# Optimization experiments

Measured on AMD Instinct MI355X. Metric: run time of the kernel, lower is better.

The kernel has to match this reference:

```python
import jax, jax.numpy as jnp
import numpy as np

MARGIN = 0.25
GAMMA = 256.0
NEG_FILL = -1e9  # finite mask value; logits are bounded by ~gamma*2.25*2, so this is safely dominated


def setup_inputs() -> dict:
    key = jax.random.key(0)
    k1, k2 = jax.random.split(key)
    embeddings = jax.random.normal(k1, (8192, 128), dtype=jnp.float32)
    labels = jax.random.randint(k2, (8192,), 0, 512)
    return {"embeddings": embeddings, "labels": labels}


def reference(embeddings, labels):
    B = embeddings.shape[0]
    # L2-normalize rows (F.normalize eps=1e-12)
    norm = jnp.maximum(jnp.linalg.norm(embeddings, axis=1, keepdims=True), 1e-12)
    e = embeddings / norm
    sim = e @ e.T  # [B, B]

    eq = labels[:, None] == labels[None, :]
    eye = jnp.eye(B, dtype=bool)
    pos_mask = eq & ~eye
    neg_mask = (~eq) & ~eye

    sim_d = jax.lax.stop_gradient(sim)  # alphas use detached similarities
    alpha_p = jnp.maximum(1.0 + MARGIN - sim_d, 0.0)
    alpha_n = jnp.maximum(sim_d + MARGIN, 0.0)

    logit_p = -GAMMA * alpha_p * (sim - (1.0 - MARGIN))
    logit_n = GAMMA * alpha_n * (sim - MARGIN)

    # masked per-row logsumexp (finite fill keeps grads clean)
    lp = jax.scipy.special.logsumexp(jnp.where(pos_mask, logit_p, NEG_FILL), axis=1)
    ln = jax.scipy.special.logsumexp(jnp.where(neg_mask, logit_n, NEG_FILL), axis=1)

    valid = pos_mask.any(axis=1) & neg_mask.any(axis=1)
    per_row = jax.nn.softplus(jnp.where(valid, lp + ln, NEG_FILL))
    per_row = jnp.where(valid, per_row, 0.0)
    n_valid = jnp.maximum(valid.sum(), 1)
    return jnp.sum(per_row) / n_valid.astype(per_row.dtype)
```

## Files before the change

### kernel.cpp

```cpp
#include <hip/hip_runtime.h>
#include <math.h>

#define NB 8192
#define ND 128
#define NT 64
#define NTRI 2080
#define NLAB 512
#define MAXM 64

typedef unsigned short u16;
typedef unsigned int u32;
typedef __attribute__((ext_vector_type(8))) short bf16x8;
typedef __attribute__((ext_vector_type(4))) float f32x4;

#define G2 369.3299304675746f
#define NEG_C (-23.083120654223414f)
#define SENT (-1e30f)
#define LN2F 0.6931471805599453f

static __device__ __forceinline__ void gload16(const void* g, void* l) {
  __builtin_amdgcn_global_load_lds(
      (const __attribute__((address_space(1))) u32*)g,
      (__attribute__((address_space(3))) u32*)l, 16, 0, 0);
}

static __device__ __forceinline__ float fexp2(float x) {
  return __builtin_amdgcn_exp2f(x);
}

static __device__ __forceinline__ u16 f2bf(float f) {
  u32 u = __float_as_uint(f);
  u32 r = (u + 0x7FFF + ((u >> 16) & 1)) >> 16;
  return (u16)r;
}

static __device__ __forceinline__ float wave_sum_f(float v) {
  #pragma unroll
  for (int off = 1; off < 64; off <<= 1) v += __shfl_xor(v, off);
  return v;
}

__global__ __launch_bounds__(512) void k_prep(const float* __restrict__ emb,
                                              u16* __restrict__ e,
                                              int* __restrict__ counters) {
  if (blockIdx.x == 0 && threadIdx.x < 2) counters[threadIdx.x] = 0;
  const int l = threadIdx.x & 63;
  const int w = threadIdx.x >> 6;
  const int row = blockIdx.x * 8 + w;
  const float2 v = reinterpret_cast<const float2*>(emb)[(size_t)row * 64 + l];
  float ss = wave_sum_f(v.x * v.x + v.y * v.y);
  const float inv = 1.0f / fmaxf(sqrtf(ss), 1e-12f);
  ushort2 o;
  o.x = f2bf(v.x * inv);
  o.y = f2bf(v.y * inv);
  reinterpret_cast<ushort2*>(e)[(size_t)row * 64 + l] = o;
}

__global__ __launch_bounds__(256, 3) void k_mainpos(const u16* __restrict__ e,
                                                    const int* __restrict__ labels,
                                                    float* __restrict__ part,
                                                    float* __restrict__ poscorr) {
  __shared__ __align__(16) char S[33792];
  const int bid = blockIdx.x;
  const int tid = threadIdx.x;
  const int l = tid & 63;
  const int w = tid >> 6;
  const int lr_ = l & 15;
  const int lg = l >> 4;

  if (bid < NTRI) {
    int ti = (int)((129.0f - sqrtf(16641.0f - 8.0f * (float)bid)) * 0.5f);
    if (ti > NT - 1) ti = NT - 1;
    if (ti < 0) ti = 0;
    #define PRE(t) ((t) * NT - ((t) * ((t) - 1)) / 2)
    while (PRE(ti + 1) <= bid) ++ti;
    while (PRE(ti) > bid) --ti;
    const int tj = ti + (bid - PRE(ti));
    #undef PRE
    const int row0 = ti * 128;
    const int col0 = tj * 128;
    const bool diag = (ti == tj);
    char* Bh[2] = { S, S + 16384 };

    bf16x8 af[2][4];
    #pragma unroll
    for (int m = 0; m < 2; ++m)
      #pragma unroll
      for (int ks = 0; ks < 4; ++ks)
        af[m][ks] = *(const bf16x8*)(e + (size_t)(row0 + w * 32 + m * 16 + lr_) * ND +
                                     ks * 32 + lg * 8);

    #pragma unroll
    for (int i = 0; i < 4; ++i) {
      const int rr = w * 16 + i * 4 + lg;
      gload16(e + (size_t)(col0 + rr) * ND + (lr_ ^ (rr & 15)) * 8,
              Bh[0] + w * 4096 + i * 1024);
    }

    float sn[8], colp[8];
    #pragma unroll
    for (int q = 0; q < 8; ++q) { sn[q] = 0.f; colp[q] = 0.f; }

    __syncthreads();

    #pragma unroll
    for (int i = 0; i < 4; ++i) {
      const int rr = w * 16 + i * 4 + lg;
      gload16(e + (size_t)(col0 + 64 + rr) * ND + (lr_ ^ (rr & 15)) * 8,
              Bh[1] + w * 4096 + i * 1024);
    }

    #pragma unroll
    for (int h = 0; h < 2; ++h) {
      f32x4 acc[2][4];
      #pragma unroll
      for (int m = 0; m < 2; ++m)
        #pragma unroll
        for (int n = 0; n < 4; ++n)
          #pragma unroll
          for (int q = 0; q < 4; ++q) acc[m][n][q] = 0.f;

      #pragma unroll
      for (int ks = 0; ks < 4; ++ks) {
        const int kslot = (ks * 4 + lg) ^ lr_;
        bf16x8 bfr[4];
        #pragma unroll
        for (int n = 0; n < 4; ++n)
          bfr[n] = *(const bf16x8*)(Bh[h] + (n * 16 + lr_) * 256 + kslot * 16);
        #pragma unroll
        for (int m = 0; m < 2; ++m)
          #pragma unroll
          for (int n = 0; n < 4; ++n)
            acc[m][n] = __builtin_amdgcn_mfma_f32_16x16x32_bf16(af[m][ks], bfr[n],
                                                                acc[m][n], 0, 0, 0);
      }

      #pragma unroll
      for (int m = 0; m < 2; ++m) {
        #pragma unroll
        for (int n = 0; n < 4; ++n) {
          const bool dmn = diag && (w * 32 + m * 16 == h * 64 + n * 16);
          float scc = 0.f;
          #pragma unroll
          for (int j = 0; j < 4; ++j) {
            const float sv = acc[m][n][j];
            float xn = fmaf(sv * sv, G2, NEG_C);
            xn = (sv > -0.25f) ? xn : 0.f;
            if (dmn) xn = (lr_ == lg * 4 + j) ? SENT : xn;
            const float ev = fexp2(xn);
            sn[m * 4 + j] += ev;
            scc += ev;
          }
          colp[h * 4 + n] += scc;
        }
      }
      if (h == 0) __syncthreads();
    }

    #pragma unroll
    for (int q = 0; q < 8; ++q) {
      #pragma unroll
      for (int off = 1; off < 16; off <<= 1) sn[q] += __shfl_xor(sn[q], off);
    }
    if (lr_ == 0) {
      #pragma unroll
      for (int m = 0; m < 2; ++m)
        #pragma unroll
        for (int j = 0; j < 4; ++j) {
          const int row = row0 + w * 32 + m * 16 + lg * 4 + j;
          part[(size_t)tj * NB + row] = sn[m * 4 + j];
        }
    }

    if (!diag) {
      #pragma unroll
      for (int q = 0; q < 8; ++q) {
        colp[q] += __shfl_xor(colp[q], 16);
        colp[q] += __shfl_xor(colp[q], 32);
      }
      __syncthreads();
      float* colbuf = (float*)S;
      if (l < 16) {
        #pragma unroll
        for (int q = 0; q < 8; ++q)
          colbuf[w * 128 + (q >> 2) * 64 + (q & 3) * 16 + lr_] = colp[q];
      }
      __syncthreads();
      if (tid < 128) {
        const float cs_ = colbuf[tid] + colbuf[128 + tid] +
                          colbuf[256 + tid] + colbuf[384 + tid];
        part[(size_t)ti * NB + col0 + tid] = cs_;
      }
    }
  } else {
    int* lab = (int*)S;
    for (int i = tid; i < NB / 4; i += 256)
      ((int4*)lab)[i] = ((const int4*)labels)[i];
    __syncthreads();

    const int L = (bid - NTRI) * 4 + w;
    int* memL = (int*)(S + 32768) + w * MAXM;

    int cnt = 0;
    for (int base = 0; base < NB; base += 64) {
      const int lv = lab[base + l];
      const unsigned long long mk = __ballot(lv == L);
      if (lv == L) {
        const int pos = __popcll(mk & ((1ull << l) - 1));
        if (cnt + pos < MAXM) memL[cnt + pos] = base + l;
      }
      cnt += __popcll(mk);
    }
    int c = cnt > MAXM ? MAXM : cnt;
    __syncthreads();

    const int nt = (c + 15) >> 4;
    for (int rb = 0; rb < nt; ++rb) {
      const int ri = rb * 16 + lr_;
      bf16x8 af[4];
      if (ri < c) {
        const u16* src = e + (size_t)memL[ri] * ND;
        #pragma unroll
        for (int ks = 0; ks < 4; ++ks)
          af[ks] = *(const bf16x8*)(src + ks * 32 + lg * 8);
      } else {
        #pragma unroll
        for (int ks = 0; ks < 4; ++ks) af[ks] = (bf16x8)0;
      }
      float corr[4], mp[4], sp[4];
      #pragma unroll
      for (int r = 0; r < 4; ++r) { corr[r] = 0.f; mp[r] = SENT; sp[r] = 0.f; }

      for (int cb = 0; cb < nt; ++cb) {
        const int ci = cb * 16 + lr_;
        bf16x8 bfr[4];
        if (ci < c) {
          const u16* src = e + (size_t)memL[ci] * ND;
          #pragma unroll
          for (int ks = 0; ks < 4; ++ks)
            bfr[ks] = *(const bf16x8*)(src + ks * 32 + lg * 8);
        } else {
          #pragma unroll
          for (int ks = 0; ks < 4; ++ks) bfr[ks] = (bf16x8)0;
        }
        f32x4 acc;
        #pragma unroll
        for (int r = 0; r < 4; ++r) acc[r] = 0.f;
        #pragma unroll
        for (int ks = 0; ks < 4; ++ks)
          acc = __builtin_amdgcn_mfma_f32_16x16x32_bf16(af[ks], bfr[ks], acc, 0, 0, 0);

        #pragma unroll
        for (int r = 0; r < 4; ++r) {
          const int R = rb * 16 + lg * 4 + r;
          const int Cj = cb * 16 + lr_;
          const bool ok = (R < c) && (Cj < c) && (R != Cj);
          const float sv = acc[r];
          float xn = fmaf(sv * sv, G2, NEG_C);
          xn = (sv > -0.25f) ? xn : 0.f;
          corr[r] += ok ? fexp2(xn) : 0.f;
          if (ok) {
            const float t1 = 1.25f - sv;
            const float xp = G2 * fmaxf(t1, 0.f) * (t1 - 0.5f);
            if (xp > mp[r]) { sp[r] = sp[r] * fexp2(mp[r] - xp) + 1.f; mp[r] = xp; }
            else sp[r] += fexp2(xp - mp[r]);
          }
        }
      }
      #pragma unroll
      for (int r = 0; r < 4; ++r) {
        #pragma unroll
        for (int off = 1; off < 16; off <<= 1) {
          corr[r] += __shfl_xor(corr[r], off);
          const float m2 = __shfl_xor(mp[r], off), s2 = __shfl_xor(sp[r], off);
          const float M = fmaxf(mp[r], m2);
          const float t1 = sp[r] * fexp2(mp[r] - M);
          const float t2 = s2 * fexp2(m2 - M);
          mp[r] = M; sp[r] = t1 + t2;
        }
      }
      if (lr_ == 0) {
        #pragma unroll
        for (int r = 0; r < 4; ++r) {
          const int R = rb * 16 + lg * 4 + r;
          if (R < c) {
            float* o = poscorr + (size_t)memL[R] * 4;
            o[0] = mp[r]; o[1] = sp[r]; o[2] = corr[r]; o[3] = (float)(c - 1);
          }
        }
      }
    }
  }
}

__global__ __launch_bounds__(256) void k_rowsfinal(const float* __restrict__ part,
                                                   const float* __restrict__ poscorr,
                                                   float* __restrict__ bsum,
                                                   int* __restrict__ counter,
                                                   float* __restrict__ out) {
  const int bid = blockIdx.x;
  const int tid = threadIdx.x;
  const int l = tid & 63, w = tid >> 6;
  const int row = bid * 256 + tid;
  float sn = 0.f;
  #pragma unroll 8
  for (int q = 0; q < NT; ++q)
    sn += part[(size_t)q * NB + row];
  const float4 pc = *reinterpret_cast<const float4*>(poscorr + (size_t)row * 4);
  const int npi = (int)(pc.w + 0.5f);
  const bool valid = (npi > 0) && (npi < NB - 1);
  float val = 0.f;
  if (valid) {
    const float snn = fmaxf(sn - pc.z, 1e-30f);
    const float lp = LN2F * (pc.x + log2f(pc.y));
    const float ln_ = LN2F * log2f(snn);
    const float x = lp + ln_;
    val = fmaxf(x, 0.f) + log1pf(expf(-fabsf(x)));
  }
  float cnt = valid ? 1.f : 0.f;
  val = wave_sum_f(val);
  cnt = wave_sum_f(cnt);
  __shared__ float svals[4], scnts[4];
  __shared__ int lastflag;
  if (l == 0) { svals[w] = val; scnts[w] = cnt; }
  __syncthreads();
  if (tid == 0) {
    bsum[bid * 2 + 0] = svals[0] + svals[1] + svals[2] + svals[3];
    bsum[bid * 2 + 1] = scnts[0] + scnts[1] + scnts[2] + scnts[3];
    __threadfence();
    const int prev = atomicAdd(counter, 1);
    lastflag = (prev == 31);
  }
  __syncthreads();
  if (lastflag && w == 0) {
    __threadfence();
    float s = 0.f, c = 0.f;
    if (l < 32) {
      volatile const float* vb = (volatile const float*)bsum;
      s = vb[l * 2];
      c = vb[l * 2 + 1];
    }
    s = wave_sum_f(s);
    c = wave_sum_f(c);
    if (l == 0) out[0] = s / fmaxf(c, 1.f);
  }
}

extern "C" void kernel_launch(void* const* d_in, const int* in_sizes, int n_in,
                              void* d_out, int out_size, void* d_ws, size_t ws_size,
                              hipStream_t stream) {
  const float* emb = (const float*)d_in[0];
  const int* labels = (const int*)d_in[1];
  float* out = (float*)d_out;
  char* ws = (char*)d_ws;

  float* part    = (float*)(ws + 0);
  float* poscorr = (float*)(ws + 2097152);
  u16*   ebf     = (u16*)  (ws + 2228224);
  float* bsum    = (float*)(ws + 4325376);
  int*   counter = (int*)  (ws + 4325632);

  k_prep<<<NB / 8, 512, 0, stream>>>(emb, ebf, counter);
  k_mainpos<<<NTRI + NLAB / 4, 256, 0, stream>>>(ebf, labels, part, poscorr);
  k_rowsfinal<<<NB / 256, 256, 0, stream>>>(part, poscorr, bsum, counter, out);
}
```

Baseline: 46.86 us.

## Fuse L2-normalization and bf16 conversion into the similarity tile kernel

Removes the separate prep kernel, so each tile block loads fp32 embeddings, normalizes them and converts to bf16 in registers before writing its B tiles to LDS. This drops one launch and the bf16 buffer round-trip, and the async global-to-LDS loads and the mid-loop barrier go away. In exchange every tile block re-reads fp32 rows (twice the bytes) and repeats the normalization work redundantly, and the counter reset becomes a memset.

Result: slower. 57.53 us (+22.8%).

```diff
diff --git a/kernel.cpp b/kernel.cpp
--- a/kernel.cpp
+++ b/kernel.cpp
@@ -18,20 +18,13 @@
 #define SENT (-1e30f)
 #define LN2F 0.6931471805599453f
 
-static __device__ __forceinline__ void gload16(const void* g, void* l) {
-  __builtin_amdgcn_global_load_lds(
-      (const __attribute__((address_space(1))) u32*)g,
-      (__attribute__((address_space(3))) u32*)l, 16, 0, 0);
-}
-
 static __device__ __forceinline__ float fexp2(float x) {
   return __builtin_amdgcn_exp2f(x);
 }
 
-static __device__ __forceinline__ u16 f2bf(float f) {
+static __device__ __forceinline__ u32 f2bf(float f) {
   u32 u = __float_as_uint(f);
-  u32 r = (u + 0x7FFF + ((u >> 16) & 1)) >> 16;
-  return (u16)r;
+  return (u + 0x7FFF + ((u >> 16) & 1)) >> 16;
 }
 
 static __device__ __forceinline__ float wave_sum_f(float v) {
@@ -40,23 +33,50 @@
   return v;
 }
 
-__global__ __launch_bounds__(512) void k_prep(const float* __restrict__ emb,
-                                              u16* __restrict__ e,
-                                              int* __restrict__ counters) {
-  if (blockIdx.x == 0 && threadIdx.x < 2) counters[threadIdx.x] = 0;
-  const int l = threadIdx.x & 63;
-  const int w = threadIdx.x >> 6;
-  const int row = blockIdx.x * 8 + w;
-  const float2 v = reinterpret_cast<const float2*>(emb)[(size_t)row * 64 + l];
-  float ss = wave_sum_f(v.x * v.x + v.y * v.y);
-  const float inv = 1.0f / fmaxf(sqrtf(ss), 1e-12f);
-  ushort2 o;
-  o.x = f2bf(v.x * inv);
-  o.y = f2bf(v.y * inv);
-  reinterpret_cast<ushort2*>(e)[(size_t)row * 64 + l] = o;
-}
-
-__global__ __launch_bounds__(256, 3) void k_mainpos(const u16* __restrict__ e,
+static __device__ __forceinline__ void load32(const float* __restrict__ src,
+                                              int g, float v[32]) {
+  #pragma unroll
+  for (int ks = 0; ks < 4; ++ks) {
+    const float4 a = *(const float4*)(src + ks * 32 + g * 8);
+    const float4 b = *(const float4*)(src + ks * 32 + g * 8 + 4);
+    v[ks * 8 + 0] = a.x; v[ks * 8 + 1] = a.y; v[ks * 8 + 2] = a.z; v[ks * 8 + 3] = a.w;
+    v[ks * 8 + 4] = b.x; v[ks * 8 + 5] = b.y; v[ks * 8 + 6] = b.z; v[ks * 8 + 7] = b.w;
+  }
+}
+
+static __device__ __forceinline__ float inv_from_ss(float ss, int o1, int o2) {
+  ss += __shfl_xor(ss, o1);
+  ss += __shfl_xor(ss, o2);
+  return 1.0f / fmaxf(sqrtf(ss), 1e-12f);
+}
+
+static __device__ __forceinline__ float ss32(const float v[32]) {
+  float ss = 0.f;
+  #pragma unroll
+  for (int j = 0; j < 32; ++j) ss = fmaf(v[j], v[j], ss);
+  return ss;
+}
+
+static __device__ __forceinline__ void norm_frags(const float* __restrict__ src,
+                                                  int g, int o1, int o2,
+                                                  bf16x8 out[4]) {
+  float v[32];
+  load32(src, g, v);
+  const float inv = inv_from_ss(ss32(v), o1, o2);
+  #pragma unroll
+  for (int ks = 0; ks < 4; ++ks) {
+    u32 wd[4];
+    #pragma unroll
+    for (int p = 0; p < 4; ++p)
+      wd[p] = f2bf(v[ks * 8 + 2 * p] * inv) | (f2bf(v[ks * 8 + 2 * p + 1] * inv) << 16);
+    bf16x8 f;
+    #pragma unroll
+    for (int p = 0; p < 4; ++p) ((u32*)&f)[p] = wd[p];
+    out[ks] = f;
+  }
+}
+
+__global__ __launch_bounds__(256, 3) void k_mainpos(const float* __restrict__ emb,
                                                     const int* __restrict__ labels,
                                                     float* __restrict__ part,
                                                     float* __restrict__ poscorr) {
@@ -80,22 +100,33 @@
     const int row0 = ti * 128;
     const int col0 = tj * 128;
     const bool diag = (ti == tj);
-    char* Bh[2] = { S, S + 16384 };
+
+    {
+      const int srow = tid >> 2;
+      const int q = tid & 3;
+      #pragma unroll
+      for (int h = 0; h < 2; ++h) {
+        const float* src = emb + (size_t)(col0 + h * 64 + srow) * ND;
+        float v[32];
+        load32(src, q, v);
+        const float inv = inv_from_ss(ss32(v), 1, 2);
+        #pragma unroll
+        for (int ks = 0; ks < 4; ++ks) {
+          uint4 wd;
+          wd.x = f2bf(v[ks * 8 + 0] * inv) | (f2bf(v[ks * 8 + 1] * inv) << 16);
+          wd.y = f2bf(v[ks * 8 + 2] * inv) | (f2bf(v[ks * 8 + 3] * inv) << 16);
+          wd.z = f2bf(v[ks * 8 + 4] * inv) | (f2bf(v[ks * 8 + 5] * inv) << 16);
+          wd.w = f2bf(v[ks * 8 + 6] * inv) | (f2bf(v[ks * 8 + 7] * inv) << 16);
+          char* dst = S + h * 16384 + srow * 256 + (((ks * 4 + q) ^ (srow & 15)) * 16);
+          *(uint4*)dst = wd;
+        }
+      }
+    }
 
     bf16x8 af[2][4];
     #pragma unroll
     for (int m = 0; m < 2; ++m)
-      #pragma unroll
-      for (int ks = 0; ks < 4; ++ks)
-        af[m][ks] = *(const bf16x8*)(e + (size_t)(row0 + w * 32 + m * 16 + lr_) * ND +
-                                     ks * 32 + lg * 8);
-
-    #pragma unroll
-    for (int i = 0; i < 4; ++i) {
-      const int rr = w * 16 + i * 4 + lg;
-      gload16(e + (size_t)(col0 + rr) * ND + (lr_ ^ (rr & 15)) * 8,
-              Bh[0] + w * 4096 + i * 1024);
-    }
+      norm_frags(emb + (size_t)(row0 + w * 32 + m * 16 + lr_) * ND, lg, 16, 32, af[m]);
 
     float sn[8], colp[8];
     #pragma unroll
@@ -104,14 +135,8 @@
     __syncthreads();
 
     #pragma unroll
-    for (int i = 0; i < 4; ++i) {
-      const int rr = w * 16 + i * 4 + lg;
-      gload16(e + (size_t)(col0 + 64 + rr) * ND + (lr_ ^ (rr & 15)) * 8,
-              Bh[1] + w * 4096 + i * 1024);
-    }
-
-    #pragma unroll
     for (int h = 0; h < 2; ++h) {
+      const char* Bh = S + h * 16384;
       f32x4 acc[2][4];
       #pragma unroll
       for (int m = 0; m < 2; ++m)
@@ -126,7 +151,7 @@
         bf16x8 bfr[4];
         #pragma unroll
         for (int n = 0; n < 4; ++n)
-          bfr[n] = *(const bf16x8*)(Bh[h] + (n * 16 + lr_) * 256 + kslot * 16);
+          bfr[n] = *(const bf16x8*)(Bh + (n * 16 + lr_) * 256 + kslot * 16);
         #pragma unroll
         for (int m = 0; m < 2; ++m)
           #pragma unroll
@@ -154,7 +179,6 @@
           colp[h * 4 + n] += scc;
         }
       }
-      if (h == 0) __syncthreads();
     }
 
     #pragma unroll
@@ -219,10 +243,7 @@
       const int ri = rb * 16 + lr_;
       bf16x8 af[4];
       if (ri < c) {
-        const u16* src = e + (size_t)memL[ri] * ND;
-        #pragma unroll
-        for (int ks = 0; ks < 4; ++ks)
-          af[ks] = *(const bf16x8*)(src + ks * 32 + lg * 8);
+        norm_frags(emb + (size_t)memL[ri] * ND, lg, 16, 32, af);
       } else {
         #pragma unroll
         for (int ks = 0; ks < 4; ++ks) af[ks] = (bf16x8)0;
@@ -235,10 +256,7 @@
         const int ci = cb * 16 + lr_;
         bf16x8 bfr[4];
         if (ci < c) {
-          const u16* src = e + (size_t)memL[ci] * ND;
-          #pragma unroll
-          for (int ks = 0; ks < 4; ++ks)
-            bfr[ks] = *(const bf16x8*)(src + ks * 32 + lg * 8);
+          norm_frags(emb + (size_t)memL[ci] * ND, lg, 16, 32, bfr);
         } else {
           #pragma unroll
           for (int ks = 0; ks < 4; ++ks) bfr[ks] = (bf16x8)0;
@@ -356,11 +374,10 @@
 
   float* part    = (float*)(ws + 0);
   float* poscorr = (float*)(ws + 2097152);
-  u16*   ebf     = (u16*)  (ws + 2228224);
-  float* bsum    = (float*)(ws + 4325376);
-  int*   counter = (int*)  (ws + 4325632);
-
-  k_prep<<<NB / 8, 512, 0, stream>>>(emb, ebf, counter);
-  k_mainpos<<<NTRI + NLAB / 4, 256, 0, stream>>>(ebf, labels, part, poscorr);
+  float* bsum    = (float*)(ws + 2228224);
+  int*   counter = (int*)  (ws + 2228480);
+
+  hipMemsetAsync(counter, 0, 8, stream);
+  k_mainpos<<<NTRI + NLAB / 4, 256, 0, stream>>>(emb, labels, part, poscorr);
   k_rowsfinal<<<NB / 256, 256, 0, stream>>>(part, poscorr, bsum, counter, out);
 }
```

## Process four triangle tiles per block with cross-tile prefetch of B and A

Applied to the files above, without the earlier changes.

Each block of the main kernel now handles four consecutive upper-triangle tiles instead of one, so the grid shrinks from 2080 to 520 tile blocks. While the second half of one tile is computed, the next tile's first B half is staged into LDS and its A fragments are loaded into a second register set. The next tile's second B half is staged after the column-sum barrier, and the column buffer moves to a dedicated LDS region. This hides global load latency and cuts per-block launch and setup cost, but it doubles the A fragment registers, lowers launch bounds occupancy from 3 to 2, and gives coarser load balance across CUs.

Result: faster. 41.60 us (-11.2%).

```diff
diff --git a/kernel.cpp b/kernel.cpp
--- a/kernel.cpp
+++ b/kernel.cpp
@@ -5,6 +5,8 @@
 #define ND 128
 #define NT 64
 #define NTRI 2080
+#define TPB 4
+#define NTRB (NTRI / TPB)
 #define NLAB 512
 #define MAXM 64
 
@@ -38,6 +40,17 @@
   #pragma unroll
   for (int off = 1; off < 64; off <<= 1) v += __shfl_xor(v, off);
   return v;
+}
+
+static __device__ __forceinline__ int pre_(int t) { return t * NT - (t * (t - 1)) / 2; }
+static __device__ __forceinline__ void trimap(int item, int& ti, int& tj) {
+  int t = (int)((129.0f - sqrtf(16641.0f - 8.0f * (float)item)) * 0.5f);
+  if (t > NT - 1) t = NT - 1;
+  if (t < 0) t = 0;
+  while (pre_(t + 1) <= item) ++t;
+  while (pre_(t) > item) --t;
+  ti = t;
+  tj = t + (item - pre_(t));
 }
 
 __global__ __launch_bounds__(512) void k_prep(const float* __restrict__ emb,
@@ -56,11 +69,61 @@
   reinterpret_cast<ushort2*>(e)[(size_t)row * 64 + l] = o;
 }
 
-__global__ __launch_bounds__(256, 3) void k_mainpos(const u16* __restrict__ e,
+#define LOADA(AF, ROW0)                                                         \
+  _Pragma("unroll")                                                             \
+  for (int m_ = 0; m_ < 2; ++m_) {                                              \
+    _Pragma("unroll")                                                           \
+    for (int ks_ = 0; ks_ < 4; ++ks_)                                           \
+      AF[m_][ks_] = *(const bf16x8*)(e + (size_t)((ROW0) + w * 32 + m_ * 16 + lr_) * ND + ks_ * 32 + lg * 8); \
+  }
+
+#define STAGEB(BUFOFF, COL0, H)                                                 \
+  _Pragma("unroll")                                                             \
+  for (int i_ = 0; i_ < 4; ++i_) {                                              \
+    const int rr_ = w * 16 + i_ * 4 + lg;                                       \
+    gload16(e + (size_t)((COL0) + (H) * 64 + rr_) * ND + (lr_ ^ (rr_ & 15)) * 8, \
+            S + (BUFOFF) + w * 4096 + i_ * 1024);                               \
+  }
+
+#define COMPUTE_HALF(AF, BUFOFF, H, ROW0, DIAG)                                 \
+  {                                                                             \
+    f32x4 acc[2][4];                                                            \
+    _Pragma("unroll") for (int m_ = 0; m_ < 2; ++m_)                            \
+      _Pragma("unroll") for (int n_ = 0; n_ < 4; ++n_)                          \
+        _Pragma("unroll") for (int q_ = 0; q_ < 4; ++q_) acc[m_][n_][q_] = 0.f; \
+    _Pragma("unroll") for (int ks_ = 0; ks_ < 4; ++ks_) {                       \
+      const int kslot_ = (ks_ * 4 + lg) ^ lr_;                                  \
+      bf16x8 bfr[4];                                                            \
+      _Pragma("unroll") for (int n_ = 0; n_ < 4; ++n_)                          \
+        bfr[n_] = *(const bf16x8*)(S + (BUFOFF) + (n_ * 16 + lr_) * 256 + kslot_ * 16); \
+      _Pragma("unroll") for (int m_ = 0; m_ < 2; ++m_)                          \
+        _Pragma("unroll") for (int n_ = 0; n_ < 4; ++n_)                        \
+          acc[m_][n_] = __builtin_amdgcn_mfma_f32_16x16x32_bf16(AF[m_][ks_], bfr[n_], acc[m_][n_], 0, 0, 0); \
+    }                                                                           \
+    _Pragma("unroll") for (int m_ = 0; m_ < 2; ++m_) {                          \
+      _Pragma("unroll") for (int n_ = 0; n_ < 4; ++n_) {                        \
+        const bool dmn_ = (DIAG) && (w * 32 + m_ * 16 == (H) * 64 + n_ * 16);   \
+        float scc_ = 0.f;                                                       \
+        _Pragma("unroll") for (int j_ = 0; j_ < 4; ++j_) {                      \
+          const float sv_ = acc[m_][n_][j_];                                    \
+          float xn_ = fmaf(sv_ * sv_, G2, NEG_C);                               \
+          xn_ = (sv_ > -0.25f) ? xn_ : 0.f;                                     \
+          if (dmn_) xn_ = (lr_ == lg * 4 + j_) ? SENT : xn_;                    \
+          const float ev_ = fexp2(xn_);                                         \
+          sn[m_ * 4 + j_] += ev_;                                               \
+          scc_ += ev_;                                                          \
+        }                                                                       \
+        colp[(H) * 4 + n_] += scc_;                                             \
+      }                                                                         \
+    }                                                                           \
+  }
+
+__global__ __launch_bounds__(256, 2) void k_mainpos(const u16* __restrict__ e,
                                                     const int* __restrict__ labels,
                                                     float* __restrict__ part,
                                                     float* __restrict__ poscorr) {
-  __shared__ __align__(16) char S[33792];
+  __shared__ __align__(16) char S[34816];
+  float* colbuf = (float*)(S + 32768);
   const int bid = blockIdx.x;
   const int tid = threadIdx.x;
   const int l = tid & 63;
@@ -68,129 +131,78 @@
   const int lr_ = l & 15;
   const int lg = l >> 4;
 
-  if (bid < NTRI) {
-    int ti = (int)((129.0f - sqrtf(16641.0f - 8.0f * (float)bid)) * 0.5f);
-    if (ti > NT - 1) ti = NT - 1;
-    if (ti < 0) ti = 0;
-    #define PRE(t) ((t) * NT - ((t) * ((t) - 1)) / 2)
-    while (PRE(ti + 1) <= bid) ++ti;
-    while (PRE(ti) > bid) --ti;
-    const int tj = ti + (bid - PRE(ti));
-    #undef PRE
-    const int row0 = ti * 128;
-    const int col0 = tj * 128;
-    const bool diag = (ti == tj);
-    char* Bh[2] = { S, S + 16384 };
-
-    bf16x8 af[2][4];
-    #pragma unroll
-    for (int m = 0; m < 2; ++m)
-      #pragma unroll
-      for (int ks = 0; ks < 4; ++ks)
-        af[m][ks] = *(const bf16x8*)(e + (size_t)(row0 + w * 32 + m * 16 + lr_) * ND +
-                                     ks * 32 + lg * 8);
-
-    #pragma unroll
-    for (int i = 0; i < 4; ++i) {
-      const int rr = w * 16 + i * 4 + lg;
-      gload16(e + (size_t)(col0 + rr) * ND + (lr_ ^ (rr & 15)) * 8,
-              Bh[0] + w * 4096 + i * 1024);
-    }
+  if (bid < NTRB) {
+    const int item0 = bid * TPB;
+    int ti, tj;
+    trimap(item0, ti, tj);
+    int row0 = ti * 128, col0 = tj * 128;
+    bool diag = (ti == tj);
+
+    bf16x8 afA[2][4], afB[2][4];
+    LOADA(afA, row0);
+    STAGEB(0, col0, 0);
 
     float sn[8], colp[8];
     #pragma unroll
     for (int q = 0; q < 8; ++q) { sn[q] = 0.f; colp[q] = 0.f; }
 
     __syncthreads();
+    STAGEB(16384, col0, 1);
 
     #pragma unroll
-    for (int i = 0; i < 4; ++i) {
-      const int rr = w * 16 + i * 4 + lg;
-      gload16(e + (size_t)(col0 + 64 + rr) * ND + (lr_ ^ (rr & 15)) * 8,
-              Bh[1] + w * 4096 + i * 1024);
-    }
-
-    #pragma unroll
-    for (int h = 0; h < 2; ++h) {
-      f32x4 acc[2][4];
-      #pragma unroll
-      for (int m = 0; m < 2; ++m)
-        #pragma unroll
-        for (int n = 0; n < 4; ++n)
-          #pragma unroll
-          for (int q = 0; q < 4; ++q) acc[m][n][q] = 0.f;
-
-      #pragma unroll
-      for (int ks = 0; ks < 4; ++ks) {
-        const int kslot = (ks * 4 + lg) ^ lr_;
-        bf16x8 bfr[4];
-        #pragma unroll
-        for (int n = 0; n < 4; ++n)
-          bfr[n] = *(const bf16x8*)(Bh[h] + (n * 16 + lr_) * 256 + kslot * 16);
+    for (int i = 0; i < TPB; ++i) {
+      int nti = 0, ntj = 0, nrow0 = 0, ncol0 = 0;
+      bool ndiag = false;
+
+      if ((i & 1) == 0) { COMPUTE_HALF(afA, 0, 0, row0, diag); }
+      else              { COMPUTE_HALF(afB, 0, 0, row0, diag); }
+      __syncthreads();
+      if (i < TPB - 1) {
+        trimap(item0 + i + 1, nti, ntj);
+        nrow0 = nti * 128; ncol0 = ntj * 128; ndiag = (nti == ntj);
+        STAGEB(0, ncol0, 0);
+        if ((i & 1) == 0) { LOADA(afB, nrow0); }
+        else              { LOADA(afA, nrow0); }
+      }
+
+      if ((i & 1) == 0) { COMPUTE_HALF(afA, 16384, 1, row0, diag); }
+      else              { COMPUTE_HALF(afB, 16384, 1, row0, diag); }
+
+      #pragma unroll
+      for (int q = 0; q < 8; ++q) {
+        #pragma unroll
+        for (int off = 1; off < 16; off <<= 1) sn[q] += __shfl_xor(sn[q], off);
+      }
+      if (lr_ == 0) {
         #pragma unroll
         for (int m = 0; m < 2; ++m)
           #pragma unroll
-          for (int n = 0; n < 4; ++n)
-            acc[m][n] = __builtin_amdgcn_mfma_f32_16x16x32_bf16(af[m][ks], bfr[n],
-                                                                acc[m][n], 0, 0, 0);
-      }
-
-      #pragma unroll
-      for (int m = 0; m < 2; ++m) {
-        #pragma unroll
-        for (int n = 0; n < 4; ++n) {
-          const bool dmn = diag && (w * 32 + m * 16 == h * 64 + n * 16);
-          float scc = 0.f;
-          #pragma unroll
           for (int j = 0; j < 4; ++j) {
-            const float sv = acc[m][n][j];
-            float xn = fmaf(sv * sv, G2, NEG_C);
-            xn = (sv > -0.25f) ? xn : 0.f;
-            if (dmn) xn = (lr_ == lg * 4 + j) ? SENT : xn;
-            const float ev = fexp2(xn);
-            sn[m * 4 + j] += ev;
-            scc += ev;
+            const int row = row0 + w * 32 + m * 16 + lg * 4 + j;
+            part[(size_t)tj * NB + row] = sn[m * 4 + j];
           }
-          colp[h * 4 + n] += scc;
-        }
-      }
-      if (h == 0) __syncthreads();
-    }
-
-    #pragma unroll
-    for (int q = 0; q < 8; ++q) {
-      #pragma unroll
-      for (int off = 1; off < 16; off <<= 1) sn[q] += __shfl_xor(sn[q], off);
-    }
-    if (lr_ == 0) {
-      #pragma unroll
-      for (int m = 0; m < 2; ++m)
-        #pragma unroll
-        for (int j = 0; j < 4; ++j) {
-          const int row = row0 + w * 32 + m * 16 + lg * 4 + j;
-          part[(size_t)tj * NB + row] = sn[m * 4 + j];
-        }
-    }
-
-    if (!diag) {
+      }
       #pragma unroll
       for (int q = 0; q < 8; ++q) {
         colp[q] += __shfl_xor(colp[q], 16);
         colp[q] += __shfl_xor(colp[q], 32);
       }
-      __syncthreads();
-      float* colbuf = (float*)S;
-      if (l < 16) {
+      if (!diag && l < 16) {
         #pragma unroll
         for (int q = 0; q < 8; ++q)
           colbuf[w * 128 + (q >> 2) * 64 + (q & 3) * 16 + lr_] = colp[q];
       }
+
       __syncthreads();
-      if (tid < 128) {
+      if (i < TPB - 1) STAGEB(16384, ncol0, 1);
+      if (!diag && tid < 128) {
         const float cs_ = colbuf[tid] + colbuf[128 + tid] +
                           colbuf[256 + tid] + colbuf[384 + tid];
         part[(size_t)ti * NB + col0 + tid] = cs_;
       }
+      #pragma unroll
+      for (int q = 0; q < 8; ++q) { sn[q] = 0.f; colp[q] = 0.f; }
+      ti = nti; tj = ntj; row0 = nrow0; col0 = ncol0; diag = ndiag;
     }
   } else {
     int* lab = (int*)S;
@@ -198,7 +210,7 @@
       ((int4*)lab)[i] = ((const int4*)labels)[i];
     __syncthreads();
 
-    const int L = (bid - NTRI) * 4 + w;
+    const int L = (bid - NTRB) * 4 + w;
     int* memL = (int*)(S + 32768) + w * MAXM;
 
     int cnt = 0;
@@ -361,6 +373,6 @@
   int*   counter = (int*)  (ws + 4325632);
 
   k_prep<<<NB / 8, 512, 0, stream>>>(emb, ebf, counter);
-  k_mainpos<<<NTRI + NLAB / 4, 256, 0, stream>>>(ebf, labels, part, poscorr);
+  k_mainpos<<<NTRB + NLAB / 4, 256, 0, stream>>>(ebf, labels, part, poscorr);
   k_rowsfinal<<<NB / 256, 256, 0, stream>>>(part, poscorr, bsum, counter, out);
 }
```
